# Optimization experiments

Hardware: AMD Instinct MI355X
Metric: run time of the kernel (lower is better)

Reference implementation:

```python
import jax, jax.numpy as jnp
import numpy as np

N_PATCH, N_Z, K, BS = 16, 128, 10, 1024
D = N_PATCH * N_Z


def setup_inputs() -> dict:
    key = jax.random.key(0)
    k1, k2, k3, k4 = jax.random.split(key, 4)
    z = jax.random.normal(k1, (BS, D), dtype=jnp.float32)
    m = jax.random.normal(k2, (K, D), dtype=jnp.float32)
    L = jax.random.normal(k3, (K, D, D), dtype=jnp.float32)
    components = jax.random.randint(k4, (BS,), 0, K, dtype=jnp.int64)
    return {"z": z, "m": m, "L": L, "components": components}


def reference(z, m, L, components):
    # samps[k] = m[k] + z @ L[k].T   -> (K, BS, D)
    samps = jnp.einsum('bd,ked->kbe', z, L) + m[:, None, :]
    # one-hot mask-and-sum over components == gather selected expert per sample
    x = samps[components, jnp.arange(z.shape[0])]  # (BS, D)
    return x.reshape(-1, N_PATCH, N_Z)
```

## Files before the change

### kernel.cpp

```cpp
#include <hip/hip_runtime.h>
#include <hip/hip_bf16.h>


#define DDIM  2048
#define BSAMP 1024
#define KCOMP 10
#define MPAD  160
#define NT    32
#define BK    32
#define NITER (DDIM / BK)
#define TILEP 12288
#define ABYTES 12288
#define BBYTES 4096
#define STAGE_BYTES (ABYTES + BBYTES)
#define NBUF  3
#define NXCD  8
#define NWG   (KCOMP * (DDIM / NT))

typedef __attribute__((ext_vector_type(8))) short bf16x8;
typedef __attribute__((ext_vector_type(4))) float f32x4;

__device__ __forceinline__ void async16(void* lds, const void* g) {
    __builtin_amdgcn_global_load_lds(
        (const __attribute__((address_space(1))) void*)g,
        (__attribute__((address_space(3))) void*)lds, 16, 0, 0);
}

__device__ __forceinline__ short bfs(float x) {
    __hip_bfloat16 h = __float2bfloat16(x);
    return *reinterpret_cast<short*>(&h);
}

__global__ void build_map(const int* __restrict__ comp,
                          int* __restrict__ rowmap,
                          int* __restrict__ counts) {
    __shared__ int sc[KCOMP];
    const int t = threadIdx.x;
    if (t < KCOMP) sc[t] = 0;
    __syncthreads();
    const int c = comp[t];
    const int r = atomicAdd(&sc[c], 1);
    if (r < MPAD) rowmap[c * MPAD + r] = t;
    __syncthreads();
    if (t < KCOMP) counts[t] = sc[t];
}

__global__ void zgather(const float* __restrict__ z,
                        const int* __restrict__ rowmap,
                        short* __restrict__ zb) {
    const int k  = blockIdx.x;
    const int sp = blockIdx.y;
    const int t  = threadIdx.x;
    const int c  = t & 7;
    const int g  = c & 3;
    const int s0 = rowmap[k * MPAD + 2 * sp]     & (BSAMP - 1);
    const int s1 = rowmap[k * MPAD + 2 * sp + 1] & (BSAMP - 1);
    const int src = (c >> 2) ? s1 : s0;
    const int swz = (c ^ (sp & 7)) * 16;
    char* kbase = (char*)zb + (size_t)k * NITER * TILEP + sp * 128 + swz;
#pragma unroll
    for (int p = 0; p < 2; ++p) {
        const int it = p * 32 + (t >> 3);
        const float* zr = z + (size_t)src * DDIM + it * BK + g * 8;
        f32x4 x = *(const f32x4*)zr;
        f32x4 y = *(const f32x4*)(zr + 4);
        bf16x8 r;
#pragma unroll
        for (int i = 0; i < 4; ++i) { r[i] = bfs(x[i]); r[4 + i] = bfs(y[i]); }
        *(bf16x8*)(kbase + (size_t)it * TILEP) = r;
    }
}

__global__ __launch_bounds__(256, 3)
void gmm_gemm(const short* __restrict__ zb,
              const float* __restrict__ mvec,
              const float* __restrict__ Lmat,
              const int* __restrict__ rowmap,
              const int* __restrict__ counts,
              float* __restrict__ out) {
    __shared__ __attribute__((aligned(16))) char smem[NBUF * STAGE_BYTES];
    const int t    = threadIdx.x;
    const int lane = t & 63;
    const int w    = t >> 6;
    const int mh   = w >> 1;
    const int nh   = w & 1;
    const int lin  = blockIdx.x;
    const int newlin = (lin & (NXCD - 1)) * (NWG / NXCD) + (lin >> 3);
    const int k    = newlin >> 6;
    const int n0   = (newlin & 63) * NT;
    const float* Lk = Lmat + (size_t)k * DDIM * DDIM;
    const char* zt  = (const char*)zb + (size_t)k * NITER * TILEP;
    const int cnt  = counts[k];

    int mtmax = (cnt - mh * 80 + 15) >> 4;
    mtmax = mtmax < 0 ? 0 : (mtmax > 5 ? 5 : mtmax);

    const int br = t >> 3,          bc = ((t & 7) ^ (br & 7)) * 4;
    const unsigned ub = (unsigned)(t & ~63) * 16;

    auto stage = [&](int bi, int it) {
        char* lb = smem + bi * STAGE_BYTES;
        const char* at = zt + (size_t)it * TILEP;
        async16(lb + ub,          at + t * 16);
        async16(lb + 4096 + ub,   at + 4096 + t * 16);
        async16(lb + 8192 + ub,   at + 8192 + t * 16);
        async16(lb + ABYTES + ub, Lk + (size_t)(n0 + br) * DDIM + it * BK + bc);
    };

    f32x4 acc[5];
#pragma unroll
    for (int mt = 0; mt < 5; ++mt) acc[mt] = (f32x4){0.f, 0.f, 0.f, 0.f};

    const int fr = lane & 15;
    const int g  = lane >> 4;
    const int rb = nh * 16 + fr;
    const int h0 = ((2 * g)     ^ (rb & 7)) * 4;
    const int h1 = ((2 * g + 1) ^ (rb & 7)) * 4;
    const int frh = fr >> 1;
    const int fra = (fr & 1) * 4 + g;
    const int abase = (mh * 40 + frh) * 128 + ((fra ^ frh) * 16);

    auto compute = [&](int bi) {
        const char* lb = smem + bi * STAGE_BYTES;
        const float* B = (const float*)(lb + ABYTES);
        f32x4 x = *(const f32x4*)(B + rb * 32 + h0);
        f32x4 y = *(const f32x4*)(B + rb * 32 + h1);
        bf16x8 bb;
#pragma unroll
        for (int i = 0; i < 4; ++i) { bb[i] = bfs(x[i]); bb[4 + i] = bfs(y[i]); }
#pragma unroll
        for (int mt = 0; mt < 5; ++mt) {
            if (mt < mtmax) {
                bf16x8 a = *(const bf16x8*)(lb + abase + mt * 1024);
                acc[mt] = __builtin_amdgcn_mfma_f32_16x16x32_bf16(a, bb, acc[mt], 0, 0, 0);
            }
        }
    };

    stage(0, 0); stage(1, 1); stage(2, 2);
    int bi = 0;
    for (int it = 0; it < NITER - 2; ++it) {
        asm volatile("s_waitcnt vmcnt(8)" ::: "memory");
        __builtin_amdgcn_s_barrier();
        compute(bi);
        __builtin_amdgcn_s_barrier();
        if (it + 3 < NITER) stage(bi, it + 3);
        bi = (bi == NBUF - 1) ? 0 : bi + 1;
    }
    asm volatile("s_waitcnt vmcnt(4)" ::: "memory");
    __builtin_amdgcn_s_barrier();
    compute(bi);
    __builtin_amdgcn_s_barrier();
    bi = (bi == NBUF - 1) ? 0 : bi + 1;
    asm volatile("s_waitcnt vmcnt(0)" ::: "memory");
    __builtin_amdgcn_s_barrier();
    compute(bi);

    const int rquad = g * 4;
    const int e  = n0 + nh * 16 + fr;
    const float mu = mvec[k * DDIM + e];
#pragma unroll
    for (int mt = 0; mt < 5; ++mt) {
        if (mt < mtmax) {
            const int sb = mh * 80 + mt * 16 + rquad;
#pragma unroll
            for (int r = 0; r < 4; ++r) {
                const int slot = sb + r;
                if (slot < cnt) {
                    const int b = rowmap[k * MPAD + slot];
                    out[(size_t)b * DDIM + e] = acc[mt][r] + mu;
                }
            }
        }
    }
}

extern "C" void kernel_launch(void* const* d_in, const int* in_sizes, int n_in,
                              void* d_out, int out_size, void* d_ws, size_t ws_size,
                              hipStream_t stream) {
    const float* z    = (const float*)d_in[0];
    const float* mvec = (const float*)d_in[1];
    const float* Lmat = (const float*)d_in[2];
    const int* comp   = (const int*)d_in[3];
    float* out        = (float*)d_out;

    int* rowmap = (int*)d_ws;
    int* counts = rowmap + KCOMP * MPAD;
    short* zb   = (short*)((char*)d_ws + 8192);

    build_map<<<1, BSAMP, 0, stream>>>(comp, rowmap, counts);
    zgather<<<dim3(KCOMP, MPAD / 2), 256, 0, stream>>>(z, rowmap, zb);
    gmm_gemm<<<NWG, 256, 0, stream>>>(zb, mvec, Lmat, rowmap, counts, out);
}
```

Before: 274.3 us.

## Load A operand directly into registers, stage only L tiles through LDS

The bf16 z tile (A operand) is no longer staged through LDS. Each wave loads its A fragments straight from global memory into registers using inline global_load_dwordx4, double-buffered as a0/a1. LDS now holds only the fp32 L tiles, triple-buffered, so shared memory per block drops and launch bounds rise to 4 blocks per CU. The manual vmcnt accounting is intricate, and A is now read redundantly by the waves that share it rather than once per block, which adds L2 traffic.

```diff
diff --git a/kernel.cpp b/kernel.cpp
--- a/kernel.cpp
+++ b/kernel.cpp
@@ -10,9 +10,7 @@
 #define BK    32
 #define NITER (DDIM / BK)
 #define TILEP 12288
-#define ABYTES 12288
 #define BBYTES 4096
-#define STAGE_BYTES (ABYTES + BBYTES)
 #define NBUF  3
 #define NXCD  8
 #define NWG   (KCOMP * (DDIM / NT))
@@ -29,6 +27,12 @@
 __device__ __forceinline__ short bfs(float x) {
     __hip_bfloat16 h = __float2bfloat16(x);
     return *reinterpret_cast<short*>(&h);
+}
+
+__device__ __forceinline__ bf16x8 gld16(const void* p) {
+    bf16x8 r;
+    asm volatile("global_load_dwordx4 %0, %1, off" : "=v"(r) : "v"(p));
+    return r;
 }
 
 __global__ void build_map(const int* __restrict__ comp,
@@ -71,14 +75,14 @@
     }
 }
 
-__global__ __launch_bounds__(256, 3)
+__global__ __launch_bounds__(256, 4)
 void gmm_gemm(const short* __restrict__ zb,
               const float* __restrict__ mvec,
               const float* __restrict__ Lmat,
               const int* __restrict__ rowmap,
               const int* __restrict__ counts,
               float* __restrict__ out) {
-    __shared__ __attribute__((aligned(16))) char smem[NBUF * STAGE_BYTES];
+    __shared__ __attribute__((aligned(16))) char smem[NBUF * BBYTES];
     const int t    = threadIdx.x;
     const int lane = t & 63;
     const int w    = t >> 6;
@@ -98,19 +102,6 @@
     const int br = t >> 3,          bc = ((t & 7) ^ (br & 7)) * 4;
     const unsigned ub = (unsigned)(t & ~63) * 16;
 
-    auto stage = [&](int bi, int it) {
-        char* lb = smem + bi * STAGE_BYTES;
-        const char* at = zt + (size_t)it * TILEP;
-        async16(lb + ub,          at + t * 16);
-        async16(lb + 4096 + ub,   at + 4096 + t * 16);
-        async16(lb + 8192 + ub,   at + 8192 + t * 16);
-        async16(lb + ABYTES + ub, Lk + (size_t)(n0 + br) * DDIM + it * BK + bc);
-    };
-
-    f32x4 acc[5];
-#pragma unroll
-    for (int mt = 0; mt < 5; ++mt) acc[mt] = (f32x4){0.f, 0.f, 0.f, 0.f};
-
     const int fr = lane & 15;
     const int g  = lane >> 4;
     const int rb = nh * 16 + fr;
@@ -118,43 +109,109 @@
     const int h1 = ((2 * g + 1) ^ (rb & 7)) * 4;
     const int frh = fr >> 1;
     const int fra = (fr & 1) * 4 + g;
-    const int abase = (mh * 40 + frh) * 128 + ((fra ^ frh) * 16);
-
-    auto compute = [&](int bi) {
-        const char* lb = smem + bi * STAGE_BYTES;
-        const float* B = (const float*)(lb + ABYTES);
+    const char* za = zt + mh * 5120 + frh * 128 + ((fra ^ frh) * 16);
+
+    f32x4 acc[5];
+#pragma unroll
+    for (int mt = 0; mt < 5; ++mt) acc[mt] = (f32x4){0.f, 0.f, 0.f, 0.f};
+
+    bf16x8 a0[5], a1[5];
+
+    auto stageB = [&](int bi, int it) {
+        async16(smem + bi * BBYTES + ub,
+                Lk + (size_t)(n0 + br) * DDIM + it * BK + bc);
+    };
+    auto loadA = [&](bf16x8 (&a)[5], int it) {
+        const char* p = za + (size_t)it * TILEP;
+#pragma unroll
+        for (int mt = 0; mt < 5; ++mt) a[mt] = gld16(p + mt * 1024);
+    };
+    auto computeB = [&](int bi) {
+        const float* B = (const float*)(smem + bi * BBYTES);
         f32x4 x = *(const f32x4*)(B + rb * 32 + h0);
         f32x4 y = *(const f32x4*)(B + rb * 32 + h1);
         bf16x8 bb;
 #pragma unroll
         for (int i = 0; i < 4; ++i) { bb[i] = bfs(x[i]); bb[4 + i] = bfs(y[i]); }
-#pragma unroll
-        for (int mt = 0; mt < 5; ++mt) {
-            if (mt < mtmax) {
-                bf16x8 a = *(const bf16x8*)(lb + abase + mt * 1024);
-                acc[mt] = __builtin_amdgcn_mfma_f32_16x16x32_bf16(a, bb, acc[mt], 0, 0, 0);
-            }
+        return bb;
+    };
+    auto mfma5 = [&](bf16x8 (&a)[5], bf16x8 bb) {
+#pragma unroll
+        for (int mt = 0; mt < 5; ++mt)
+            if (mt < mtmax)
+                acc[mt] = __builtin_amdgcn_mfma_f32_16x16x32_bf16(a[mt], bb, acc[mt], 0, 0, 0);
+    };
+
+    stageB(0, 0); loadA(a0, 0); stageB(1, 1); loadA(a1, 1); stageB(2, 2);
+
+    int bi = 0;
+    for (int j = 0; j < 60; j += 2) {
+        asm volatile("s_waitcnt vmcnt(12)" ::: "memory");
+        __builtin_amdgcn_s_barrier();
+        {
+            bf16x8 bb = computeB(bi);
+            asm volatile("s_waitcnt vmcnt(6)" ::: "memory");
+            __builtin_amdgcn_sched_barrier(0);
+            mfma5(a0, bb);
         }
-    };
-
-    stage(0, 0); stage(1, 1); stage(2, 2);
-    int bi = 0;
-    for (int it = 0; it < NITER - 2; ++it) {
-        asm volatile("s_waitcnt vmcnt(8)" ::: "memory");
-        __builtin_amdgcn_s_barrier();
-        compute(bi);
-        __builtin_amdgcn_s_barrier();
-        if (it + 3 < NITER) stage(bi, it + 3);
+        loadA(a0, j + 2);
+        __builtin_amdgcn_s_barrier();
+        stageB(bi, j + 3);
         bi = (bi == NBUF - 1) ? 0 : bi + 1;
-    }
-    asm volatile("s_waitcnt vmcnt(4)" ::: "memory");
-    __builtin_amdgcn_s_barrier();
-    compute(bi);
-    __builtin_amdgcn_s_barrier();
+        asm volatile("s_waitcnt vmcnt(12)" ::: "memory");
+        __builtin_amdgcn_s_barrier();
+        {
+            bf16x8 bb = computeB(bi);
+            asm volatile("s_waitcnt vmcnt(6)" ::: "memory");
+            __builtin_amdgcn_sched_barrier(0);
+            mfma5(a1, bb);
+        }
+        loadA(a1, j + 3);
+        __builtin_amdgcn_s_barrier();
+        stageB(bi, j + 4);
+        bi = (bi == NBUF - 1) ? 0 : bi + 1;
+    }
+    asm volatile("s_waitcnt vmcnt(12)" ::: "memory");
+    __builtin_amdgcn_s_barrier();
+    {
+        bf16x8 bb = computeB(bi);
+        asm volatile("s_waitcnt vmcnt(6)" ::: "memory");
+        __builtin_amdgcn_sched_barrier(0);
+        mfma5(a0, bb);
+    }
+    loadA(a0, 62);
+    __builtin_amdgcn_s_barrier();
+    stageB(bi, 63);
     bi = (bi == NBUF - 1) ? 0 : bi + 1;
-    asm volatile("s_waitcnt vmcnt(0)" ::: "memory");
-    __builtin_amdgcn_s_barrier();
-    compute(bi);
+    asm volatile("s_waitcnt vmcnt(12)" ::: "memory");
+    __builtin_amdgcn_s_barrier();
+    {
+        bf16x8 bb = computeB(bi);
+        asm volatile("s_waitcnt vmcnt(6)" ::: "memory");
+        __builtin_amdgcn_sched_barrier(0);
+        mfma5(a1, bb);
+    }
+    loadA(a1, 63);
+    __builtin_amdgcn_s_barrier();
+    bi = (bi == NBUF - 1) ? 0 : bi + 1;
+    asm volatile("s_waitcnt vmcnt(11)" ::: "memory");
+    __builtin_amdgcn_s_barrier();
+    {
+        bf16x8 bb = computeB(bi);
+        asm volatile("s_waitcnt vmcnt(6)" ::: "memory");
+        __builtin_amdgcn_sched_barrier(0);
+        mfma5(a0, bb);
+    }
+    __builtin_amdgcn_s_barrier();
+    bi = (bi == NBUF - 1) ? 0 : bi + 1;
+    asm volatile("s_waitcnt vmcnt(5)" ::: "memory");
+    __builtin_amdgcn_s_barrier();
+    {
+        bf16x8 bb = computeB(bi);
+        asm volatile("s_waitcnt vmcnt(0)" ::: "memory");
+        __builtin_amdgcn_sched_barrier(0);
+        mfma5(a1, bb);
+    }
 
     const int rquad = g * 4;
     const int e  = n0 + nh * 16 + fr;
```

New measurement: 273.1 us. About the same (-0.5%).
